# Optimization experiments

Hardware: AMD Instinct MI355X
Metric: run time of the kernel (lower is better)

The kernel has to match this reference:

```python
import jax, jax.numpy as jnp
import numpy as np

B, C, H, W = 2, 128, 48, 48
NUM_HEADS = 8


def dct_matrix(N):
    # Orthonormal DCT-II matrix: D[k, n] = s_k * cos(pi * (n + 0.5) * k / N)
    n = np.arange(N)
    D = np.cos(np.pi * (n[None, :] + 0.5) * n[:, None] / N) * np.sqrt(2.0 / N)
    D[0] *= 1.0 / np.sqrt(2.0)
    return jnp.asarray(D, dtype=jnp.float32)


def setup_inputs() -> dict:
    key = jax.random.key(0)
    ks = jax.random.split(key, 10)
    w_scale = 1.0 / np.sqrt(C)  # kaiming-ish init for 1x1 convs
    inp = {
        "freq_feat": jax.random.normal(ks[0], (B, C, H, W), dtype=jnp.float32),
        "spatial_feat": jax.random.normal(ks[1], (B, C, H, W), dtype=jnp.float32),
        "Wq": jax.random.normal(ks[2], (C, C), dtype=jnp.float32) * w_scale,
        "bq": jnp.zeros((C,), dtype=jnp.float32),
        "Wk": jax.random.normal(ks[3], (C, C), dtype=jnp.float32) * w_scale,
        "bk": jnp.zeros((C,), dtype=jnp.float32),
        "Wv": jax.random.normal(ks[4], (C, C), dtype=jnp.float32) * w_scale,
        "bv": jnp.zeros((C,), dtype=jnp.float32),
        "Wo": jax.random.normal(ks[5], (C, C), dtype=jnp.float32) * w_scale,
        "bo": jnp.zeros((C,), dtype=jnp.float32),
    }
    return inp


def _proj(x, Wm, b):
    # 1x1 conv == channel-mixing GEMM
    return jnp.einsum('oc,bchw->bohw', Wm, x) + b[None, :, None, None]


def reference(freq_feat, spatial_feat, Wq, bq, Wk, bk, Wv, bv, Wo, bo):
    b, c, h, w = freq_feat.shape
    nh = NUM_HEADS
    d = c // nh
    L = h * w

    # 2D orthonormal DCT-II of the spatial features
    DH = dct_matrix(h)
    DW = dct_matrix(w)
    spatial_freq = jnp.einsum('hm,bcmn,wn->bchw', DH, spatial_feat, DW)

    Q = _proj(freq_feat, Wq, bq)
    K = _proj(spatial_freq, Wk, bk)
    V = _proj(spatial_freq, Wv, bv)

    # (B, C, H, W) -> (B, nh, L, d)
    def to_heads(x):
        return x.reshape(b, nh, d, L).transpose(0, 1, 3, 2)

    Qh, Kh, Vh = to_heads(Q), to_heads(K), to_heads(V)

    scale = 1.0 / np.sqrt(d)
    scores = jnp.einsum('bhld,bhsd->bhls', Qh, Kh) * scale  # (B, nh, L, L)
    attn = jax.nn.softmax(scores, axis=-1)
    out = jnp.einsum('bhls,bhsd->bhld', attn, Vh)  # (B, nh, L, d)

    out = out.transpose(0, 1, 3, 2).reshape(b, c, h, w)
    return _proj(out, Wo, bo)
```

## Files before the change

### kernel.cpp

```cpp
#include <hip/hip_runtime.h>
#include <math.h>

#define L_TOT 2304
#define C_TOT 128
#define KSCALE 0.36067376022224085f

#if __has_builtin(__builtin_amdgcn_exp2f)
#define EXP2(x) __builtin_amdgcn_exp2f(x)
#else
#define EXP2(x) __expf(0.69314718055994531f * (x))
#endif

typedef float v4f  __attribute__((ext_vector_type(4)));
typedef __bf16 v8bf __attribute__((ext_vector_type(8)));
typedef __bf16 v4bf __attribute__((ext_vector_type(4)));

#define MFMA_16x16x32_BF16(A, B, C) __builtin_amdgcn_mfma_f32_16x16x32_bf16((A), (B), (C), 0, 0, 0)

__device__ __forceinline__ void async_cp16(const __bf16* g, __bf16* l){
  __builtin_amdgcn_global_load_lds((const __attribute__((address_space(1))) unsigned int*)g,
                                   (__attribute__((address_space(3))) unsigned int*)l,
                                   16, 0, 0);
}

#if __has_builtin(__builtin_amdgcn_permlane32_swap)
__device__ __forceinline__ void pl32swap(unsigned &a, unsigned &b){
  auto r = __builtin_amdgcn_permlane32_swap((int)a, (int)b, false, false);
  a = (unsigned)r[0]; b = (unsigned)r[1];
}
#else
__device__ __forceinline__ void pl32swap(unsigned &a, unsigned &b){
  asm volatile("v_permlane32_swap_b32 %0, %1" : "+v"(a), "+v"(b));
}
#endif
#if __has_builtin(__builtin_amdgcn_permlane16_swap)
__device__ __forceinline__ void pl16swap(unsigned &a, unsigned &b){
  auto r = __builtin_amdgcn_permlane16_swap((int)a, (int)b, false, false);
  a = (unsigned)r[0]; b = (unsigned)r[1];
}
#else
__device__ __forceinline__ void pl16swap(unsigned &a, unsigned &b){
  asm volatile("v_permlane16_swap_b32 %0, %1" : "+v"(a), "+v"(b));
}
#endif

template<int MODE>
__device__ __forceinline__ void mfma_proj(const float* __restrict__ W,
                                          const float* __restrict__ bias,
                                          const float* __restrict__ Xb,
                                          __bf16* __restrict__ Yh,
                                          float scale, float bscale,
                                          int n0, __bf16* Bhi, int tid){
  __bf16* Blo = Bhi + 4352;
  const int wave = tid >> 6, lane = tid & 63, qd = lane >> 4, cn = lane & 15;
  const int m0 = wave * 32;
  v8bf ahi[2][4], alo[2][4];
  #pragma unroll
  for (int rt = 0; rt < 2; rt++)
    #pragma unroll
    for (int ks = 0; ks < 4; ks++){
      const float* wp = W + (size_t)(m0 + rt * 16 + cn) * C_TOT + ks * 32 + qd * 8;
      float4 w0 = *(const float4*)wp;
      float4 w1 = *(const float4*)(wp + 4);
      float wv[8] = {w0.x, w0.y, w0.z, w0.w, w1.x, w1.y, w1.z, w1.w};
      #pragma unroll
      for (int j = 0; j < 8; j++){
        __bf16 h = (__bf16)wv[j];
        ahi[rt][ks][j] = h;
        alo[rt][ks][j] = (__bf16)(wv[j] - (float)h);
      }
    }
  {
    int k = tid >> 1, nh = tid & 1;
    const float* xp = Xb + (size_t)k * L_TOT + n0 + nh * 16;
    float4 x0 = *(const float4*)xp;
    float4 x1 = *(const float4*)(xp + 4);
    float4 x2 = *(const float4*)(xp + 8);
    float4 x3 = *(const float4*)(xp + 12);
    float xv[16] = {x0.x, x0.y, x0.z, x0.w, x1.x, x1.y, x1.z, x1.w,
                    x2.x, x2.y, x2.z, x2.w, x3.x, x3.y, x3.z, x3.w};
    #pragma unroll
    for (int i = 0; i < 16; i++){
      __bf16 h = (__bf16)xv[i];
      int row = nh * 16 + i;
      Bhi[row * 136 + k] = h;
      Blo[row * 136 + k] = (__bf16)(xv[i] - (float)h);
    }
  }
  __syncthreads();
  v4f acc[2][2];
  #pragma unroll
  for (int rt = 0; rt < 2; rt++)
    #pragma unroll
    for (int ct = 0; ct < 2; ct++) acc[rt][ct] = (v4f){0.f, 0.f, 0.f, 0.f};
  #pragma unroll
  for (int ks = 0; ks < 4; ks++){
    v8bf bhi[2], blo[2];
    #pragma unroll
    for (int ct = 0; ct < 2; ct++){
      bhi[ct] = *(const v8bf*)&Bhi[(ct * 16 + cn) * 136 + ks * 32 + qd * 8];
      blo[ct] = *(const v8bf*)&Blo[(ct * 16 + cn) * 136 + ks * 32 + qd * 8];
    }
    #pragma unroll
    for (int rt = 0; rt < 2; rt++)
      #pragma unroll
      for (int ct = 0; ct < 2; ct++){
        acc[rt][ct] = MFMA_16x16x32_BF16(ahi[rt][ks], bhi[ct], acc[rt][ct]);
        acc[rt][ct] = MFMA_16x16x32_BF16(ahi[rt][ks], blo[ct], acc[rt][ct]);
        acc[rt][ct] = MFMA_16x16x32_BF16(alo[rt][ks], bhi[ct], acc[rt][ct]);
      }
  }
  #pragma unroll
  for (int rt = 0; rt < 2; rt++){
    float bv[4];
    #pragma unroll
    for (int r = 0; r < 4; r++) bv[r] = bias[m0 + rt * 16 + qd * 4 + r] * bscale;
    #pragma unroll
    for (int ct = 0; ct < 2; ct++){
      int col = n0 + ct * 16 + cn;
      if (MODE == 1){
        v4bf kk;
        #pragma unroll
        for (int r = 0; r < 4; r++) kk[r] = (__bf16)((acc[rt][ct][r] + bv[r]) * scale);
        *(v4bf*)&Yh[(size_t)col * C_TOT + m0 + rt * 16 + qd * 4] = kk;
      } else {
        #pragma unroll
        for (int r = 0; r < 4; r++)
          Yh[(size_t)(m0 + rt * 16 + qd * 4 + r) * L_TOT + col] = (__bf16)(acc[rt][ct][r] + bv[r]);
      }
    }
  }
}

__global__ __launch_bounds__(256) void k_q_dct(
    const float* __restrict__ freq, const float* __restrict__ spat,
    const float* __restrict__ Wq, const float* __restrict__ bq,
    __bf16* __restrict__ QT, float* __restrict__ SF){
  __shared__ __align__(16) unsigned char smraw[34560];
  int tid = threadIdx.x;
  if (blockIdx.x < 144){
    int idx = blockIdx.x;
    int b = idx / 72, n0 = (idx % 72) * 32;
    size_t off = (size_t)b * C_TOT * L_TOT;
    mfma_proj<1>(Wq, bq, freq + off, QT + (size_t)b * L_TOT * C_TOT, 1.0f, 1.0f, n0, (__bf16*)smraw, tid);
    return;
  }
  int img = blockIdx.x - 144;
  __bf16* Xhi = (__bf16*)smraw;
  __bf16* Xlo = Xhi + 3456;
  __bf16* Dm  = Xhi + 6912;
  __bf16* Thi = Xhi + 10368;
  __bf16* Tlo = Xhi + 13824;
  const float* src = spat + (size_t)img * 2304;
  for (int i = tid; i < 8640; i += 256) ((unsigned int*)smraw)[i] = 0u;
  __syncthreads();
  for (int i = tid; i < 2304; i += 256){
    int a = i / 48, n = i - a * 48;
    int m = ((2 * n + 1) * a) % 192;
    float v = cosf(0.032724923474893679f * (float)m) * 0.204124145231931508f;
    if (a == 0) v *= 0.707106781186547524f;
    Dm[a * 72 + n] = (__bf16)v;
  }
  for (int i = tid; i < 2304; i += 256){
    int mm = i / 48, n = i - mm * 48;
    float v = src[i];
    __bf16 h = (__bf16)v;
    Xhi[mm * 72 + n] = h;
    Xlo[mm * 72 + n] = (__bf16)(v - (float)h);
  }
  __syncthreads();
  int wave = tid >> 6, lane = tid & 63, qd = lane >> 4, cn = lane & 15;
  for (int t = wave; t < 9; t += 4){
    int mi = t / 3, wi = t - mi * 3;
    v8bf ah0 = *(const v8bf*)&Xhi[(mi * 16 + cn) * 72 + qd * 8];
    v8bf ah1 = *(const v8bf*)&Xhi[(mi * 16 + cn) * 72 + 32 + qd * 8];
    v8bf al0 = *(const v8bf*)&Xlo[(mi * 16 + cn) * 72 + qd * 8];
    v8bf al1 = *(const v8bf*)&Xlo[(mi * 16 + cn) * 72 + 32 + qd * 8];
    v8bf b0 = *(const v8bf*)&Dm[(wi * 16 + cn) * 72 + qd * 8];
    v8bf b1 = *(const v8bf*)&Dm[(wi * 16 + cn) * 72 + 32 + qd * 8];
    v4f acc = (v4f){0.f, 0.f, 0.f, 0.f};
    acc = MFMA_16x16x32_BF16(ah0, b0, acc);
    acc = MFMA_16x16x32_BF16(ah1, b1, acc);
    acc = MFMA_16x16x32_BF16(al0, b0, acc);
    acc = MFMA_16x16x32_BF16(al1, b1, acc);
    v4bf th, tl;
    #pragma unroll
    for (int r = 0; r < 4; r++){
      __bf16 h = (__bf16)acc[r];
      th[r] = h;
      tl[r] = (__bf16)(acc[r] - (float)h);
    }
    *(v4bf*)&Thi[(wi * 16 + cn) * 72 + mi * 16 + qd * 4] = th;
    *(v4bf*)&Tlo[(wi * 16 + cn) * 72 + mi * 16 + qd * 4] = tl;
  }
  __syncthreads();
  float* dst = SF + (size_t)img * 2304;
  for (int t = wave; t < 9; t += 4){
    int hi_ = t / 3, wi = t - hi_ * 3;
    v8bf a0 = *(const v8bf*)&Dm[(hi_ * 16 + cn) * 72 + qd * 8];
    v8bf a1 = *(const v8bf*)&Dm[(hi_ * 16 + cn) * 72 + 32 + qd * 8];
    v8bf bh0 = *(const v8bf*)&Thi[(wi * 16 + cn) * 72 + qd * 8];
    v8bf bh1 = *(const v8bf*)&Thi[(wi * 16 + cn) * 72 + 32 + qd * 8];
    v8bf bl0 = *(const v8bf*)&Tlo[(wi * 16 + cn) * 72 + qd * 8];
    v8bf bl1 = *(const v8bf*)&Tlo[(wi * 16 + cn) * 72 + 32 + qd * 8];
    v4f acc = (v4f){0.f, 0.f, 0.f, 0.f};
    acc = MFMA_16x16x32_BF16(a0, bh0, acc);
    acc = MFMA_16x16x32_BF16(a1, bh1, acc);
    acc = MFMA_16x16x32_BF16(a0, bl0, acc);
    acc = MFMA_16x16x32_BF16(a1, bl1, acc);
    int w = wi * 16 + cn;
    #pragma unroll
    for (int r = 0; r < 4; r++)
      dst[(size_t)(hi_ * 16 + qd * 4 + r) * 48 + w] = acc[r];
  }
}

__global__ __launch_bounds__(256) void k_kv(
    const float* __restrict__ SF,
    const float* __restrict__ Wk, const float* __restrict__ bk,
    const float* __restrict__ Wv, const float* __restrict__ bv,
    __bf16* __restrict__ KT, __bf16* __restrict__ Vg){
  __shared__ __align__(16) unsigned char smraw[17408];
  int job = blockIdx.x / 144;
  int idx = blockIdx.x % 144;
  int b = idx / 72, n0 = (idx % 72) * 32;
  size_t off = (size_t)b * C_TOT * L_TOT;
  if (job == 0)
    mfma_proj<1>(Wk, bk, SF + off, KT + (size_t)b * L_TOT * C_TOT, KSCALE, 1.0f, n0, (__bf16*)smraw, threadIdx.x);
  else
    mfma_proj<2>(Wv, bv, SF + off, Vg + off, 1.0f, 1.0f, n0, (__bf16*)smraw, threadIdx.x);
}

__global__ __launch_bounds__(256) void k_attn(const __bf16* __restrict__ QT,
                                              const __bf16* __restrict__ KT,
                                              const __bf16* __restrict__ V,
                                              __bf16* __restrict__ AO){
  const int L = L_TOT;
  int bh = blockIdx.y;
  int b = bh >> 3, h = bh & 7;
  int c0 = h * 16;
  const __bf16* QTb = QT + (size_t)b * L * C_TOT;
  const __bf16* KTb = KT + (size_t)b * L * C_TOT;
  const __bf16* Vb  = V  + ((size_t)b * C_TOT + c0) * L;
  int tid = threadIdx.x;
  int wave = tid >> 6, lane = tid & 63;
  int qd = lane >> 4, cn = lane & 15;
  int l0 = blockIdx.x * 48;

  __shared__ __align__(16) __bf16 smem[8192 + 8192];
  __bf16* Kt = smem;
  __bf16* Vs = smem + 8192;

  v8bf qf[3];
  #pragma unroll
  for (int t = 0; t < 3; t++){
    #pragma unroll
    for (int j = 0; j < 8; j++) qf[t][j] = (__bf16)0.0f;
  }
  if (qd < 2){
    #pragma unroll
    for (int t = 0; t < 3; t++)
      qf[t] = *(const v8bf*)&QTb[(size_t)(l0 + t * 16 + cn) * C_TOT + c0 + qd * 8];
  }

  v4f acc[3];
  float den[3] = {0.f, 0.f, 0.f};
  #pragma unroll
  for (int t = 0; t < 3; t++) acc[t] = (v4f){0.f, 0.f, 0.f, 0.f};

  for (int ch = 0; ch < 5; ch++){
    int s0 = ch * 512;
    int cnt = (ch == 4) ? 256 : 512;
    __syncthreads();
    {
      int per = (cnt >> 5) >> 2;
      for (int jj = 0; jj < per; jj++){
        int j = wave * per + jj;
        int s = j * 32 + (lane >> 1);
        async_cp16(KTb + (size_t)(s0 + s) * C_TOT + c0 + (lane & 1) * 8,
                   Kt + j * 512);
      }
      if (cnt == 512){
        #pragma unroll
        for (int jj = 0; jj < 4; jj++){
          int d = wave * 4 + jj;
          async_cp16(Vb + (size_t)d * L + s0 + ((lane ^ (d & 7)) << 3),
                     Vs + d * 512);
        }
      } else {
        int d = tid >> 4, og = tid & 15;
        const __bf16* gp = Vb + (size_t)d * L + s0 + og * 16;
        v8bf v0 = *(const v8bf*)gp;
        v8bf v1 = *(const v8bf*)(gp + 8);
        int pd = d & 7;
        *(v8bf*)&Vs[d * 512 + (((og * 2)     ^ pd) << 3)] = v0;
        *(v8bf*)&Vs[d * 512 + (((og * 2 + 1) ^ pd) << 3)] = v1;
      }
    }
    __syncthreads();

    int nsu = cnt >> 7;
    int wbase = wave * (cnt >> 2);
    for (int su = 0; su < nsu; su++){
      int sb = wbase + su * 32;
      v8bf a0, a1;
      #pragma unroll
      for (int j = 0; j < 8; j++){ a0[j] = (__bf16)0.0f; a1[j] = (__bf16)0.0f; }
      if (qd < 2){
        a0 = *(const v8bf*)&Kt[(sb + cn) * 16 + qd * 8];
        a1 = *(const v8bf*)&Kt[(sb + 16 + cn) * 16 + qd * 8];
      }
      int jv = sb >> 3;
      v8bf vf = *(const v8bf*)&Vs[cn * 512 + (((jv + qd) ^ (cn & 7)) << 3)];
      #pragma unroll
      for (int t = 0; t < 3; t++){
        v4f z = {0.f, 0.f, 0.f, 0.f};
        v4f st0 = MFMA_16x16x32_BF16(a0, qf[t], z);
        v4f st1 = MFMA_16x16x32_BF16(a1, qf[t], z);
        float p0[4], p1[4];
        #pragma unroll
        for (int i = 0; i < 4; i++){
          p0[i] = EXP2(st0[i]); den[t] += p0[i];
          p1[i] = EXP2(st1[i]); den[t] += p1[i];
        }
        v4bf cc0, cc1;
        #pragma unroll
        for (int i = 0; i < 4; i++){ cc0[i] = (__bf16)p0[i]; cc1[i] = (__bf16)p1[i]; }
        unsigned U0 = ((unsigned*)&cc0)[0], U1 = ((unsigned*)&cc0)[1];
        unsigned U2 = ((unsigned*)&cc1)[0], U3 = ((unsigned*)&cc1)[1];
        pl32swap(U0, U2); pl32swap(U1, U3);
        pl16swap(U0, U2); pl16swap(U1, U3);
        v8bf pf;
        ((unsigned*)&pf)[0] = U0; ((unsigned*)&pf)[1] = U1;
        ((unsigned*)&pf)[2] = U2; ((unsigned*)&pf)[3] = U3;
        acc[t] = MFMA_16x16x32_BF16(vf, pf, acc[t]);
      }
    }
  }

  __syncthreads();
  float* redA = (float*)smem;
  float* redD = (float*)smem + 3072;
  #pragma unroll
  for (int t = 0; t < 3; t++){
    *(v4f*)&redA[((wave * 3 + t) * 64 + lane) * 4] = acc[t];
    redD[(wave * 3 + t) * 64 + lane] = den[t];
  }
  __syncthreads();
  if (wave < 3){
    int t = wave;
    v4f a = (v4f){0.f, 0.f, 0.f, 0.f};
    float dn = 0.f;
    #pragma unroll
    for (int w2 = 0; w2 < 4; w2++){
      v4f xx = *(const v4f*)&redA[((w2 * 3 + t) * 64 + lane) * 4];
      a[0] += xx[0]; a[1] += xx[1]; a[2] += xx[2]; a[3] += xx[3];
      dn += redD[(w2 * 3 + t) * 64 + lane];
    }
    dn += __shfl_xor(dn, 16);
    dn += __shfl_xor(dn, 32);
    float inv = 1.0f / dn;
    __bf16* Ao = AO + ((size_t)b * C_TOT + c0) * L;
    #pragma unroll
    for (int r2 = 0; r2 < 4; r2++)
      Ao[(size_t)(qd * 4 + r2) * L + l0 + t * 16 + cn] = (__bf16)(a[r2] * inv);
  }
}

__global__ __launch_bounds__(256) void k_oproj(const __bf16* __restrict__ AO,
                                               const float* __restrict__ Wo, const float* __restrict__ bo,
                                               float* __restrict__ out){
  __shared__ __align__(16) __bf16 Bs[32 * 136];
  int b = blockIdx.y, n0 = blockIdx.x * 32;
  int tid = threadIdx.x;
  const int wave = tid >> 6, lane = tid & 63, qd = lane >> 4, cn = lane & 15;
  const int m0 = wave * 32;
  v8bf ahi[2][4], alo[2][4];
  #pragma unroll
  for (int rt = 0; rt < 2; rt++)
    #pragma unroll
    for (int ks = 0; ks < 4; ks++){
      const float* wp = Wo + (size_t)(m0 + rt * 16 + cn) * C_TOT + ks * 32 + qd * 8;
      float4 w0 = *(const float4*)wp;
      float4 w1 = *(const float4*)(wp + 4);
      float wv[8] = {w0.x, w0.y, w0.z, w0.w, w1.x, w1.y, w1.z, w1.w};
      #pragma unroll
      for (int j = 0; j < 8; j++){
        __bf16 h = (__bf16)wv[j];
        ahi[rt][ks][j] = h;
        alo[rt][ks][j] = (__bf16)(wv[j] - (float)h);
      }
    }
  {
    int k = tid >> 1, nh = tid & 1;
    const __bf16* src = AO + ((size_t)b * C_TOT + k) * L_TOT + n0 + nh * 16;
    v8bf x0 = *(const v8bf*)src;
    v8bf x1 = *(const v8bf*)(src + 8);
    #pragma unroll
    for (int i = 0; i < 8; i++){
      Bs[(nh * 16 + i) * 136 + k] = x0[i];
      Bs[(nh * 16 + 8 + i) * 136 + k] = x1[i];
    }
  }
  __syncthreads();
  v4f acc[2][2];
  #pragma unroll
  for (int rt = 0; rt < 2; rt++)
    #pragma unroll
    for (int ct = 0; ct < 2; ct++) acc[rt][ct] = (v4f){0.f, 0.f, 0.f, 0.f};
  #pragma unroll
  for (int ks = 0; ks < 4; ks++){
    v8bf bf[2];
    #pragma unroll
    for (int ct = 0; ct < 2; ct++)
      bf[ct] = *(const v8bf*)&Bs[(ct * 16 + cn) * 136 + ks * 32 + qd * 8];
    #pragma unroll
    for (int rt = 0; rt < 2; rt++)
      #pragma unroll
      for (int ct = 0; ct < 2; ct++){
        acc[rt][ct] = MFMA_16x16x32_BF16(ahi[rt][ks], bf[ct], acc[rt][ct]);
        acc[rt][ct] = MFMA_16x16x32_BF16(alo[rt][ks], bf[ct], acc[rt][ct]);
      }
  }
  float* ob = out + (size_t)b * C_TOT * L_TOT;
  #pragma unroll
  for (int rt = 0; rt < 2; rt++){
    float bv[4];
    #pragma unroll
    for (int r = 0; r < 4; r++) bv[r] = bo[m0 + rt * 16 + qd * 4 + r];
    #pragma unroll
    for (int ct = 0; ct < 2; ct++){
      int col = n0 + ct * 16 + cn;
      #pragma unroll
      for (int r = 0; r < 4; r++)
        ob[(size_t)(m0 + rt * 16 + qd * 4 + r) * L_TOT + col] = acc[rt][ct][r] + bv[r];
    }
  }
}

extern "C" void kernel_launch(void* const* d_in, const int* in_sizes, int n_in,
                              void* d_out, int out_size, void* d_ws, size_t ws_size,
                              hipStream_t stream){
  const float* freq = (const float*)d_in[0];
  const float* spat = (const float*)d_in[1];
  const float* Wq = (const float*)d_in[2]; const float* bq = (const float*)d_in[3];
  const float* Wk = (const float*)d_in[4]; const float* bk = (const float*)d_in[5];
  const float* Wv = (const float*)d_in[6]; const float* bv = (const float*)d_in[7];
  const float* Wo = (const float*)d_in[8]; const float* bo = (const float*)d_in[9];
  __bf16* base = (__bf16*)d_ws;

  __bf16* QTg = base;
  __bf16* KTg = base + 589824;
  __bf16* Vg  = base + 1179648;
  __bf16* AOg = base + 1769472;
  float*  SFg = (float*)(base + 2359296);
  float* out = (float*)d_out;

  k_q_dct<<<dim3(400), dim3(256), 0, stream>>>(freq, spat, Wq, bq, QTg, SFg);
  k_kv<<<dim3(288), dim3(256), 0, stream>>>(SFg, Wk, bk, Wv, bv, KTg, Vg);
  k_attn<<<dim3(48, 16), dim3(256), 0, stream>>>(QTg, KTg, Vg, AOg);
  k_oproj<<<dim3(72, 2), dim3(256), 0, stream>>>(AOg, Wo, bo, out);
}
```

Measured before the change: 115.8 us.

## Fuse all stages into one persistent kernel with grid barriers

Replaces the four separate launches (Q projection plus DCT, K/V projection, attention, output projection) with a single 768-block kernel. Stages are separated by atomic-counter grid barriers, and per-tile counters let the last attention block that finishes a column group run the output projection for it. The intent is to remove launch overhead and the inter-kernel drain/fill gaps. In exchange it needs all 768 blocks to be co-resident, which the launch bounds ask for at 3 blocks per CU, or it deadlocks. It also adds a memset and spin-wait costs.

Result: slower. 334.8 us (+189.2%).

```diff
diff --git a/kernel.cpp b/kernel.cpp
--- a/kernel.cpp
+++ b/kernel.cpp
@@ -43,6 +43,16 @@
   asm volatile("v_permlane16_swap_b32 %0, %1" : "+v"(a), "+v"(b));
 }
 #endif
+
+__device__ __forceinline__ void gbar(unsigned* c, unsigned target){
+  __syncthreads();
+  if (threadIdx.x == 0){
+    __hip_atomic_fetch_add(c, 1u, __ATOMIC_RELEASE, __HIP_MEMORY_SCOPE_AGENT);
+    while (__hip_atomic_load(c, __ATOMIC_ACQUIRE, __HIP_MEMORY_SCOPE_AGENT) < target)
+      __builtin_amdgcn_s_sleep(8);
+  }
+  __syncthreads();
+}
 
 template<int MODE>
 __device__ __forceinline__ void mfma_proj(const float* __restrict__ W,
@@ -132,26 +142,14 @@
   }
 }
 
-__global__ __launch_bounds__(256) void k_q_dct(
-    const float* __restrict__ freq, const float* __restrict__ spat,
-    const float* __restrict__ Wq, const float* __restrict__ bq,
-    __bf16* __restrict__ QT, float* __restrict__ SF){
-  __shared__ __align__(16) unsigned char smraw[34560];
-  int tid = threadIdx.x;
-  if (blockIdx.x < 144){
-    int idx = blockIdx.x;
-    int b = idx / 72, n0 = (idx % 72) * 32;
-    size_t off = (size_t)b * C_TOT * L_TOT;
-    mfma_proj<1>(Wq, bq, freq + off, QT + (size_t)b * L_TOT * C_TOT, 1.0f, 1.0f, n0, (__bf16*)smraw, tid);
-    return;
-  }
-  int img = blockIdx.x - 144;
+__device__ __forceinline__ void dct_img(const float* __restrict__ src,
+                                        float* __restrict__ dst,
+                                        unsigned char* smraw, int tid){
   __bf16* Xhi = (__bf16*)smraw;
   __bf16* Xlo = Xhi + 3456;
   __bf16* Dm  = Xhi + 6912;
   __bf16* Thi = Xhi + 10368;
   __bf16* Tlo = Xhi + 13824;
-  const float* src = spat + (size_t)img * 2304;
   for (int i = tid; i < 8640; i += 256) ((unsigned int*)smraw)[i] = 0u;
   __syncthreads();
   for (int i = tid; i < 2304; i += 256){
@@ -194,7 +192,6 @@
     *(v4bf*)&Tlo[(wi * 16 + cn) * 72 + mi * 16 + qd * 4] = tl;
   }
   __syncthreads();
-  float* dst = SF + (size_t)img * 2304;
   for (int t = wave; t < 9; t += 4){
     int hi_ = t / 3, wi = t - hi_ * 3;
     v8bf a0 = *(const v8bf*)&Dm[(hi_ * 16 + cn) * 72 + qd * 8];
@@ -215,41 +212,126 @@
   }
 }
 
-__global__ __launch_bounds__(256) void k_kv(
-    const float* __restrict__ SF,
+__device__ __forceinline__ void oproj_dev(const __bf16* __restrict__ AO,
+                                          const float* __restrict__ Wo,
+                                          const float* __restrict__ bo,
+                                          float* __restrict__ out,
+                                          int b, int n0, __bf16* Bs, int tid){
+  __syncthreads();
+  const int wave = tid >> 6, lane = tid & 63, qd = lane >> 4, cn = lane & 15;
+  const int m0 = wave * 32;
+  v8bf ahi[2][4], alo[2][4];
+  #pragma unroll
+  for (int rt = 0; rt < 2; rt++)
+    #pragma unroll
+    for (int ks = 0; ks < 4; ks++){
+      const float* wp = Wo + (size_t)(m0 + rt * 16 + cn) * C_TOT + ks * 32 + qd * 8;
+      float4 w0 = *(const float4*)wp;
+      float4 w1 = *(const float4*)(wp + 4);
+      float wv[8] = {w0.x, w0.y, w0.z, w0.w, w1.x, w1.y, w1.z, w1.w};
+      #pragma unroll
+      for (int j = 0; j < 8; j++){
+        __bf16 h = (__bf16)wv[j];
+        ahi[rt][ks][j] = h;
+        alo[rt][ks][j] = (__bf16)(wv[j] - (float)h);
+      }
+    }
+  {
+    int k = tid >> 1, nh = tid & 1;
+    const __bf16* src = AO + ((size_t)b * C_TOT + k) * L_TOT + n0 + nh * 16;
+    v8bf x0 = *(const v8bf*)src;
+    v8bf x1 = *(const v8bf*)(src + 8);
+    #pragma unroll
+    for (int i = 0; i < 8; i++){
+      Bs[(nh * 16 + i) * 136 + k] = x0[i];
+      Bs[(nh * 16 + 8 + i) * 136 + k] = x1[i];
+    }
+  }
+  __syncthreads();
+  v4f acc[2][2];
+  #pragma unroll
+  for (int rt = 0; rt < 2; rt++)
+    #pragma unroll
+    for (int ct = 0; ct < 2; ct++) acc[rt][ct] = (v4f){0.f, 0.f, 0.f, 0.f};
+  #pragma unroll
+  for (int ks = 0; ks < 4; ks++){
+    v8bf bf[2];
+    #pragma unroll
+    for (int ct = 0; ct < 2; ct++)
+      bf[ct] = *(const v8bf*)&Bs[(ct * 16 + cn) * 136 + ks * 32 + qd * 8];
+    #pragma unroll
+    for (int rt = 0; rt < 2; rt++)
+      #pragma unroll
+      for (int ct = 0; ct < 2; ct++){
+        acc[rt][ct] = MFMA_16x16x32_BF16(ahi[rt][ks], bf[ct], acc[rt][ct]);
+        acc[rt][ct] = MFMA_16x16x32_BF16(alo[rt][ks], bf[ct], acc[rt][ct]);
+      }
+  }
+  float* ob = out + (size_t)b * C_TOT * L_TOT;
+  #pragma unroll
+  for (int rt = 0; rt < 2; rt++){
+    float bv[4];
+    #pragma unroll
+    for (int r = 0; r < 4; r++) bv[r] = bo[m0 + rt * 16 + qd * 4 + r];
+    #pragma unroll
+    for (int ct = 0; ct < 2; ct++){
+      int col = n0 + ct * 16 + cn;
+      #pragma unroll
+      for (int r = 0; r < 4; r++)
+        ob[(size_t)(m0 + rt * 16 + qd * 4 + r) * L_TOT + col] = acc[rt][ct][r] + bv[r];
+    }
+  }
+}
+
+__global__ __launch_bounds__(256, 3) void k_mega(
+    const float* __restrict__ freq, const float* __restrict__ spat,
+    const float* __restrict__ Wq, const float* __restrict__ bq,
     const float* __restrict__ Wk, const float* __restrict__ bk,
     const float* __restrict__ Wv, const float* __restrict__ bv,
-    __bf16* __restrict__ KT, __bf16* __restrict__ Vg){
-  __shared__ __align__(16) unsigned char smraw[17408];
-  int job = blockIdx.x / 144;
-  int idx = blockIdx.x % 144;
-  int b = idx / 72, n0 = (idx % 72) * 32;
-  size_t off = (size_t)b * C_TOT * L_TOT;
-  if (job == 0)
-    mfma_proj<1>(Wk, bk, SF + off, KT + (size_t)b * L_TOT * C_TOT, KSCALE, 1.0f, n0, (__bf16*)smraw, threadIdx.x);
-  else
-    mfma_proj<2>(Wv, bv, SF + off, Vg + off, 1.0f, 1.0f, n0, (__bf16*)smraw, threadIdx.x);
-}
-
-__global__ __launch_bounds__(256) void k_attn(const __bf16* __restrict__ QT,
-                                              const __bf16* __restrict__ KT,
-                                              const __bf16* __restrict__ V,
-                                              __bf16* __restrict__ AO){
+    const float* __restrict__ Wo, const float* __restrict__ bo,
+    __bf16* __restrict__ QT, __bf16* __restrict__ KT, __bf16* __restrict__ Vg,
+    __bf16* __restrict__ AO, float* __restrict__ SF,
+    unsigned* __restrict__ cnt, float* __restrict__ out){
+  __shared__ __align__(16) unsigned char SMEM[34816];
+  __shared__ int oflag[2];
+  const int bid = blockIdx.x, tid = threadIdx.x;
+
+  if (bid < 144){
+    int b = bid / 72, n0 = (bid % 72) * 32;
+    size_t off = (size_t)b * C_TOT * L_TOT;
+    mfma_proj<1>(Wq, bq, freq + off, QT + (size_t)b * L_TOT * C_TOT,
+                 1.0f, 1.0f, n0, (__bf16*)SMEM, tid);
+  } else if (bid < 400){
+    int img = bid - 144;
+    dct_img(spat + (size_t)img * 2304, SF + (size_t)img * 2304, SMEM, tid);
+  }
+  gbar(&cnt[0], 768u);
+
+  if (bid < 288){
+    int job = bid / 144, idx = bid % 144;
+    int b = idx / 72, n0 = (idx % 72) * 32;
+    size_t off = (size_t)b * C_TOT * L_TOT;
+    if (job == 0)
+      mfma_proj<1>(Wk, bk, SF + off, KT + (size_t)b * L_TOT * C_TOT,
+                   KSCALE, 1.0f, n0, (__bf16*)SMEM, tid);
+    else
+      mfma_proj<2>(Wv, bv, SF + off, Vg + off, 1.0f, 1.0f, n0, (__bf16*)SMEM, tid);
+  }
+  gbar(&cnt[1], 768u);
+
   const int L = L_TOT;
-  int bh = blockIdx.y;
-  int b = bh >> 3, h = bh & 7;
-  int c0 = h * 16;
+  const int l0b = bid % 48, bh = bid / 48;
+  const int b = bh >> 3, h = bh & 7;
+  const int c0 = h * 16;
   const __bf16* QTb = QT + (size_t)b * L * C_TOT;
   const __bf16* KTb = KT + (size_t)b * L * C_TOT;
-  const __bf16* Vb  = V  + ((size_t)b * C_TOT + c0) * L;
-  int tid = threadIdx.x;
-  int wave = tid >> 6, lane = tid & 63;
-  int qd = lane >> 4, cn = lane & 15;
-  int l0 = blockIdx.x * 48;
-
-  __shared__ __align__(16) __bf16 smem[8192 + 8192];
-  __bf16* Kt = smem;
-  __bf16* Vs = smem + 8192;
+  const __bf16* Vb  = Vg + ((size_t)b * C_TOT + c0) * L;
+  const int wave = tid >> 6, lane = tid & 63;
+  const int qd = lane >> 4, cn = lane & 15;
+  const int l0 = l0b * 48;
+
+  __bf16* Kt = (__bf16*)SMEM;
+  __bf16* Vs = (__bf16*)SMEM + 8192;
 
   v8bf qf[3];
   #pragma unroll
@@ -270,17 +352,17 @@
 
   for (int ch = 0; ch < 5; ch++){
     int s0 = ch * 512;
-    int cnt = (ch == 4) ? 256 : 512;
+    int cnt_k = (ch == 4) ? 256 : 512;
     __syncthreads();
     {
-      int per = (cnt >> 5) >> 2;
+      int per = (cnt_k >> 5) >> 2;
       for (int jj = 0; jj < per; jj++){
         int j = wave * per + jj;
         int s = j * 32 + (lane >> 1);
         async_cp16(KTb + (size_t)(s0 + s) * C_TOT + c0 + (lane & 1) * 8,
                    Kt + j * 512);
       }
-      if (cnt == 512){
+      if (cnt_k == 512){
         #pragma unroll
         for (int jj = 0; jj < 4; jj++){
           int d = wave * 4 + jj;
@@ -299,8 +381,8 @@
     }
     __syncthreads();
 
-    int nsu = cnt >> 7;
-    int wbase = wave * (cnt >> 2);
+    int nsu = cnt_k >> 7;
+    int wbase = wave * (cnt_k >> 2);
     for (int su = 0; su < nsu; su++){
       int sb = wbase + su * 32;
       v8bf a0, a1;
@@ -339,8 +421,8 @@
   }
 
   __syncthreads();
-  float* redA = (float*)smem;
-  float* redD = (float*)smem + 3072;
+  float* redA = (float*)SMEM;
+  float* redD = (float*)SMEM + 3072;
   #pragma unroll
   for (int t = 0; t < 3; t++){
     *(v4f*)&redA[((wave * 3 + t) * 64 + lane) * 4] = acc[t];
@@ -365,76 +447,26 @@
     for (int r2 = 0; r2 < 4; r2++)
       Ao[(size_t)(qd * 4 + r2) * L + l0 + t * 16 + cn] = (__bf16)(a[r2] * inv);
   }
-}
-
-__global__ __launch_bounds__(256) void k_oproj(const __bf16* __restrict__ AO,
-                                               const float* __restrict__ Wo, const float* __restrict__ bo,
-                                               float* __restrict__ out){
-  __shared__ __align__(16) __bf16 Bs[32 * 136];
-  int b = blockIdx.y, n0 = blockIdx.x * 32;
-  int tid = threadIdx.x;
-  const int wave = tid >> 6, lane = tid & 63, qd = lane >> 4, cn = lane & 15;
-  const int m0 = wave * 32;
-  v8bf ahi[2][4], alo[2][4];
-  #pragma unroll
-  for (int rt = 0; rt < 2; rt++)
-    #pragma unroll
-    for (int ks = 0; ks < 4; ks++){
-      const float* wp = Wo + (size_t)(m0 + rt * 16 + cn) * C_TOT + ks * 32 + qd * 8;
-      float4 w0 = *(const float4*)wp;
-      float4 w1 = *(const float4*)(wp + 4);
-      float wv[8] = {w0.x, w0.y, w0.z, w0.w, w1.x, w1.y, w1.z, w1.w};
-      #pragma unroll
-      for (int j = 0; j < 8; j++){
-        __bf16 h = (__bf16)wv[j];
-        ahi[rt][ks][j] = h;
-        alo[rt][ks][j] = (__bf16)(wv[j] - (float)h);
-      }
-    }
-  {
-    int k = tid >> 1, nh = tid & 1;
-    const __bf16* src = AO + ((size_t)b * C_TOT + k) * L_TOT + n0 + nh * 16;
-    v8bf x0 = *(const v8bf*)src;
-    v8bf x1 = *(const v8bf*)(src + 8);
-    #pragma unroll
-    for (int i = 0; i < 8; i++){
-      Bs[(nh * 16 + i) * 136 + k] = x0[i];
-      Bs[(nh * 16 + 8 + i) * 136 + k] = x1[i];
-    }
-  }
-  __syncthreads();
-  v4f acc[2][2];
-  #pragma unroll
-  for (int rt = 0; rt < 2; rt++)
-    #pragma unroll
-    for (int ct = 0; ct < 2; ct++) acc[rt][ct] = (v4f){0.f, 0.f, 0.f, 0.f};
-  #pragma unroll
-  for (int ks = 0; ks < 4; ks++){
-    v8bf bf[2];
-    #pragma unroll
-    for (int ct = 0; ct < 2; ct++)
-      bf[ct] = *(const v8bf*)&Bs[(ct * 16 + cn) * 136 + ks * 32 + qd * 8];
-    #pragma unroll
-    for (int rt = 0; rt < 2; rt++)
-      #pragma unroll
-      for (int ct = 0; ct < 2; ct++){
-        acc[rt][ct] = MFMA_16x16x32_BF16(ahi[rt][ks], bf[ct], acc[rt][ct]);
-        acc[rt][ct] = MFMA_16x16x32_BF16(alo[rt][ks], bf[ct], acc[rt][ct]);
-      }
-  }
-  float* ob = out + (size_t)b * C_TOT * L_TOT;
-  #pragma unroll
-  for (int rt = 0; rt < 2; rt++){
-    float bv[4];
-    #pragma unroll
-    for (int r = 0; r < 4; r++) bv[r] = bo[m0 + rt * 16 + qd * 4 + r];
-    #pragma unroll
-    for (int ct = 0; ct < 2; ct++){
-      int col = n0 + ct * 16 + cn;
-      #pragma unroll
-      for (int r = 0; r < 4; r++)
-        ob[(size_t)(m0 + rt * 16 + qd * 4 + r) * L_TOT + col] = acc[rt][ct][r] + bv[r];
-    }
+
+  __syncthreads();
+  if (tid == 0){
+    int g0 = (3 * l0b) >> 1;
+    oflag[0] = -1; oflag[1] = -1;
+    #pragma unroll
+    for (int k = 0; k < 2; k++){
+      int g = g0 + k;
+      unsigned tgt = ((g % 3) == 1) ? 16u : 8u;
+      unsigned old = __hip_atomic_fetch_add(&cnt[2 + b * 72 + g], 1u,
+                                            __ATOMIC_ACQ_REL, __HIP_MEMORY_SCOPE_AGENT);
+      if (old + 1u == tgt) oflag[k] = g;
+    }
+  }
+  __syncthreads();
+  #pragma unroll
+  for (int k = 0; k < 2; k++){
+    int g = oflag[k];
+    if (g >= 0)
+      oproj_dev(AO, Wo, bo, out, b, g * 32, (__bf16*)SMEM, tid);
   }
 }
 
@@ -454,10 +486,10 @@
   __bf16* Vg  = base + 1179648;
   __bf16* AOg = base + 1769472;
   float*  SFg = (float*)(base + 2359296);
+  unsigned* cnt = (unsigned*)((char*)d_ws + 7340032);
   float* out = (float*)d_out;
 
-  k_q_dct<<<dim3(400), dim3(256), 0, stream>>>(freq, spat, Wq, bq, QTg, SFg);
-  k_kv<<<dim3(288), dim3(256), 0, stream>>>(SFg, Wk, bk, Wv, bv, KTg, Vg);
-  k_attn<<<dim3(48, 16), dim3(256), 0, stream>>>(QTg, KTg, Vg, AOg);
-  k_oproj<<<dim3(72, 2), dim3(256), 0, stream>>>(AOg, Wo, bo, out);
-}
+  hipMemsetAsync(cnt, 0, 1024, stream);
+  k_mega<<<dim3(768), dim3(256), 0, stream>>>(freq, spat, Wq, bq, Wk, bk, Wv, bv,
+                                              Wo, bo, QTg, KTg, Vg, AOg, SFg, cnt, out);
+}
```

## Fuse output projection into attention kernel via atomic completion counters

Applied to the files above, without the earlier changes.

Removes the separate output-projection launch. Each attention block increments per-column-group atomic counters once it has written its AO tile. The last block to finish a 32-column group then runs the output projection for that group in its epilogue. The counters are zeroed in the first kernel. This saves a kernel launch and its tail, but it adds atomics, extra serial work for the finishing blocks, and relies on acquire/release ordering for the AO data to be visible.

Result: slower. 155.6 us (+34.4%).

```diff
diff --git a/kernel.cpp b/kernel.cpp
--- a/kernel.cpp
+++ b/kernel.cpp
@@ -135,9 +135,11 @@
 __global__ __launch_bounds__(256) void k_q_dct(
     const float* __restrict__ freq, const float* __restrict__ spat,
     const float* __restrict__ Wq, const float* __restrict__ bq,
-    __bf16* __restrict__ QT, float* __restrict__ SF){
+    __bf16* __restrict__ QT, float* __restrict__ SF,
+    unsigned* __restrict__ cnt){
   __shared__ __align__(16) unsigned char smraw[34560];
   int tid = threadIdx.x;
+  if (blockIdx.x == 0 && tid < 160) cnt[tid] = 0u;
   if (blockIdx.x < 144){
     int idx = blockIdx.x;
     int b = idx / 72, n0 = (idx % 72) * 32;
@@ -231,10 +233,85 @@
     mfma_proj<2>(Wv, bv, SF + off, Vg + off, 1.0f, 1.0f, n0, (__bf16*)smraw, threadIdx.x);
 }
 
+__device__ __forceinline__ void oproj_dev(const __bf16* __restrict__ AO,
+                                          const float* __restrict__ Wo,
+                                          const float* __restrict__ bo,
+                                          float* __restrict__ out,
+                                          int b, int n0, __bf16* Bs, int tid){
+  __syncthreads();
+  const int wave = tid >> 6, lane = tid & 63, qd = lane >> 4, cn = lane & 15;
+  const int m0 = wave * 32;
+  v8bf ahi[2][4], alo[2][4];
+  #pragma unroll
+  for (int rt = 0; rt < 2; rt++)
+    #pragma unroll
+    for (int ks = 0; ks < 4; ks++){
+      const float* wp = Wo + (size_t)(m0 + rt * 16 + cn) * C_TOT + ks * 32 + qd * 8;
+      float4 w0 = *(const float4*)wp;
+      float4 w1 = *(const float4*)(wp + 4);
+      float wv[8] = {w0.x, w0.y, w0.z, w0.w, w1.x, w1.y, w1.z, w1.w};
+      #pragma unroll
+      for (int j = 0; j < 8; j++){
+        __bf16 h = (__bf16)wv[j];
+        ahi[rt][ks][j] = h;
+        alo[rt][ks][j] = (__bf16)(wv[j] - (float)h);
+      }
+    }
+  {
+    int k = tid >> 1, nh = tid & 1;
+    const __bf16* src = AO + ((size_t)b * C_TOT + k) * L_TOT + n0 + nh * 16;
+    v8bf x0 = *(const v8bf*)src;
+    v8bf x1 = *(const v8bf*)(src + 8);
+    #pragma unroll
+    for (int i = 0; i < 8; i++){
+      Bs[(nh * 16 + i) * 136 + k] = x0[i];
+      Bs[(nh * 16 + 8 + i) * 136 + k] = x1[i];
+    }
+  }
+  __syncthreads();
+  v4f acc[2][2];
+  #pragma unroll
+  for (int rt = 0; rt < 2; rt++)
+    #pragma unroll
+    for (int ct = 0; ct < 2; ct++) acc[rt][ct] = (v4f){0.f, 0.f, 0.f, 0.f};
+  #pragma unroll
+  for (int ks = 0; ks < 4; ks++){
+    v8bf bf[2];
+    #pragma unroll
+    for (int ct = 0; ct < 2; ct++)
+      bf[ct] = *(const v8bf*)&Bs[(ct * 16 + cn) * 136 + ks * 32 + qd * 8];
+    #pragma unroll
+    for (int rt = 0; rt < 2; rt++)
+      #pragma unroll
+      for (int ct = 0; ct < 2; ct++){
+        acc[rt][ct] = MFMA_16x16x32_BF16(ahi[rt][ks], bf[ct], acc[rt][ct]);
+        acc[rt][ct] = MFMA_16x16x32_BF16(alo[rt][ks], bf[ct], acc[rt][ct]);
+      }
+  }
+  float* ob = out + (size_t)b * C_TOT * L_TOT;
+  #pragma unroll
+  for (int rt = 0; rt < 2; rt++){
+    float bv[4];
+    #pragma unroll
+    for (int r = 0; r < 4; r++) bv[r] = bo[m0 + rt * 16 + qd * 4 + r];
+    #pragma unroll
+    for (int ct = 0; ct < 2; ct++){
+      int col = n0 + ct * 16 + cn;
+      #pragma unroll
+      for (int r = 0; r < 4; r++)
+        ob[(size_t)(m0 + rt * 16 + qd * 4 + r) * L_TOT + col] = acc[rt][ct][r] + bv[r];
+    }
+  }
+}
+
 __global__ __launch_bounds__(256) void k_attn(const __bf16* __restrict__ QT,
                                               const __bf16* __restrict__ KT,
                                               const __bf16* __restrict__ V,
-                                              __bf16* __restrict__ AO){
+                                              __bf16* __restrict__ AO,
+                                              const float* __restrict__ Wo,
+                                              const float* __restrict__ bo,
+                                              unsigned* __restrict__ cnt,
+                                              float* __restrict__ out){
   const int L = L_TOT;
   int bh = blockIdx.y;
   int b = bh >> 3, h = bh & 7;
@@ -245,9 +322,11 @@
   int tid = threadIdx.x;
   int wave = tid >> 6, lane = tid & 63;
   int qd = lane >> 4, cn = lane & 15;
-  int l0 = blockIdx.x * 48;
+  int l0b = blockIdx.x;
+  int l0 = l0b * 48;
 
   __shared__ __align__(16) __bf16 smem[8192 + 8192];
+  __shared__ int oflag[2];
   __bf16* Kt = smem;
   __bf16* Vs = smem + 8192;
 
@@ -270,17 +349,17 @@
 
   for (int ch = 0; ch < 5; ch++){
     int s0 = ch * 512;
-    int cnt = (ch == 4) ? 256 : 512;
+    int cnt_k = (ch == 4) ? 256 : 512;
     __syncthreads();
     {
-      int per = (cnt >> 5) >> 2;
+      int per = (cnt_k >> 5) >> 2;
       for (int jj = 0; jj < per; jj++){
         int j = wave * per + jj;
         int s = j * 32 + (lane >> 1);
         async_cp16(KTb + (size_t)(s0 + s) * C_TOT + c0 + (lane & 1) * 8,
                    Kt + j * 512);
       }
-      if (cnt == 512){
+      if (cnt_k == 512){
         #pragma unroll
         for (int jj = 0; jj < 4; jj++){
           int d = wave * 4 + jj;
@@ -299,8 +378,8 @@
     }
     __syncthreads();
 
-    int nsu = cnt >> 7;
-    int wbase = wave * (cnt >> 2);
+    int nsu = cnt_k >> 7;
+    int wbase = wave * (cnt_k >> 2);
     for (int su = 0; su < nsu; su++){
       int sb = wbase + su * 32;
       v8bf a0, a1;
@@ -365,76 +444,26 @@
     for (int r2 = 0; r2 < 4; r2++)
       Ao[(size_t)(qd * 4 + r2) * L + l0 + t * 16 + cn] = (__bf16)(a[r2] * inv);
   }
-}
-
-__global__ __launch_bounds__(256) void k_oproj(const __bf16* __restrict__ AO,
-                                               const float* __restrict__ Wo, const float* __restrict__ bo,
-                                               float* __restrict__ out){
-  __shared__ __align__(16) __bf16 Bs[32 * 136];
-  int b = blockIdx.y, n0 = blockIdx.x * 32;
-  int tid = threadIdx.x;
-  const int wave = tid >> 6, lane = tid & 63, qd = lane >> 4, cn = lane & 15;
-  const int m0 = wave * 32;
-  v8bf ahi[2][4], alo[2][4];
-  #pragma unroll
-  for (int rt = 0; rt < 2; rt++)
-    #pragma unroll
-    for (int ks = 0; ks < 4; ks++){
-      const float* wp = Wo + (size_t)(m0 + rt * 16 + cn) * C_TOT + ks * 32 + qd * 8;
-      float4 w0 = *(const float4*)wp;
-      float4 w1 = *(const float4*)(wp + 4);
-      float wv[8] = {w0.x, w0.y, w0.z, w0.w, w1.x, w1.y, w1.z, w1.w};
-      #pragma unroll
-      for (int j = 0; j < 8; j++){
-        __bf16 h = (__bf16)wv[j];
-        ahi[rt][ks][j] = h;
-        alo[rt][ks][j] = (__bf16)(wv[j] - (float)h);
-      }
-    }
-  {
-    int k = tid >> 1, nh = tid & 1;
-    const __bf16* src = AO + ((size_t)b * C_TOT + k) * L_TOT + n0 + nh * 16;
-    v8bf x0 = *(const v8bf*)src;
-    v8bf x1 = *(const v8bf*)(src + 8);
-    #pragma unroll
-    for (int i = 0; i < 8; i++){
-      Bs[(nh * 16 + i) * 136 + k] = x0[i];
-      Bs[(nh * 16 + 8 + i) * 136 + k] = x1[i];
-    }
-  }
-  __syncthreads();
-  v4f acc[2][2];
-  #pragma unroll
-  for (int rt = 0; rt < 2; rt++)
-    #pragma unroll
-    for (int ct = 0; ct < 2; ct++) acc[rt][ct] = (v4f){0.f, 0.f, 0.f, 0.f};
-  #pragma unroll
-  for (int ks = 0; ks < 4; ks++){
-    v8bf bf[2];
-    #pragma unroll
-    for (int ct = 0; ct < 2; ct++)
-      bf[ct] = *(const v8bf*)&Bs[(ct * 16 + cn) * 136 + ks * 32 + qd * 8];
-    #pragma unroll
-    for (int rt = 0; rt < 2; rt++)
-      #pragma unroll
-      for (int ct = 0; ct < 2; ct++){
-        acc[rt][ct] = MFMA_16x16x32_BF16(ahi[rt][ks], bf[ct], acc[rt][ct]);
-        acc[rt][ct] = MFMA_16x16x32_BF16(alo[rt][ks], bf[ct], acc[rt][ct]);
-      }
-  }
-  float* ob = out + (size_t)b * C_TOT * L_TOT;
-  #pragma unroll
-  for (int rt = 0; rt < 2; rt++){
-    float bv[4];
-    #pragma unroll
-    for (int r = 0; r < 4; r++) bv[r] = bo[m0 + rt * 16 + qd * 4 + r];
-    #pragma unroll
-    for (int ct = 0; ct < 2; ct++){
-      int col = n0 + ct * 16 + cn;
-      #pragma unroll
-      for (int r = 0; r < 4; r++)
-        ob[(size_t)(m0 + rt * 16 + qd * 4 + r) * L_TOT + col] = acc[rt][ct][r] + bv[r];
-    }
+
+  __syncthreads();
+  if (tid == 0){
+    int g0 = (3 * l0b) >> 1;
+    oflag[0] = -1; oflag[1] = -1;
+    #pragma unroll
+    for (int k = 0; k < 2; k++){
+      int g = g0 + k;
+      unsigned tgt = ((g % 3) == 1) ? 16u : 8u;
+      unsigned old = __hip_atomic_fetch_add(&cnt[2 + b * 72 + g], 1u,
+                                            __ATOMIC_ACQ_REL, __HIP_MEMORY_SCOPE_AGENT);
+      if (old + 1u == tgt) oflag[k] = g;
+    }
+  }
+  __syncthreads();
+  #pragma unroll
+  for (int k = 0; k < 2; k++){
+    int g = oflag[k];
+    if (g >= 0)
+      oproj_dev(AO, Wo, bo, out, b, g * 32, (__bf16*)smem, tid);
   }
 }
 
@@ -454,10 +483,10 @@
   __bf16* Vg  = base + 1179648;
   __bf16* AOg = base + 1769472;
   float*  SFg = (float*)(base + 2359296);
+  unsigned* cnt = (unsigned*)((char*)d_ws + 7340032);
   float* out = (float*)d_out;
 
-  k_q_dct<<<dim3(400), dim3(256), 0, stream>>>(freq, spat, Wq, bq, QTg, SFg);
+  k_q_dct<<<dim3(400), dim3(256), 0, stream>>>(freq, spat, Wq, bq, QTg, SFg, cnt);
   k_kv<<<dim3(288), dim3(256), 0, stream>>>(SFg, Wk, bk, Wv, bv, KTg, Vg);
-  k_attn<<<dim3(48, 16), dim3(256), 0, stream>>>(QTg, KTg, Vg, AOg);
-  k_oproj<<<dim3(72, 2), dim3(256), 0, stream>>>(AOg, Wo, bo, out);
-}
+  k_attn<<<dim3(48, 16), dim3(256), 0, stream>>>(QTg, KTg, Vg, AOg, Wo, bo, cnt, out);
+}
```

## Double-buffer K/V chunks in attention kernel to overlap loads with MFMA

Applied to the files above, without the earlier changes.

Replaces the five single-buffered 512-key chunks with nine 256-key chunks held in two shared-memory buffers. While one chunk is being computed, the next K chunk is fetched asynchronously and the next V chunk is loaded into registers, then written to shared memory after the compute. This drops one barrier per chunk and hides global-load latency behind the exp/MFMA work. The cost is smaller chunks, more loop iterations, and more register pressure from holding the prefetched V values.

New measurement: 113.6 us. No clear change (-1.9%).

```diff
diff --git a/kernel.cpp b/kernel.cpp
--- a/kernel.cpp
+++ b/kernel.cpp
@@ -247,9 +247,7 @@
   int qd = lane >> 4, cn = lane & 15;
   int l0 = blockIdx.x * 48;
 
-  __shared__ __align__(16) __bf16 smem[8192 + 8192];
-  __bf16* Kt = smem;
-  __bf16* Vs = smem + 8192;
+  __shared__ __align__(16) __bf16 smem[16384];
 
   v8bf qf[3];
   #pragma unroll
@@ -268,40 +266,46 @@
   #pragma unroll
   for (int t = 0; t < 3; t++) acc[t] = (v4f){0.f, 0.f, 0.f, 0.f};
 
-  for (int ch = 0; ch < 5; ch++){
-    int s0 = ch * 512;
-    int cnt = (ch == 4) ? 256 : 512;
-    __syncthreads();
-    {
-      int per = (cnt >> 5) >> 2;
-      for (int jj = 0; jj < per; jj++){
-        int j = wave * per + jj;
+  const int vd = tid >> 4, vog = tid & 15, vpd = vd & 7;
+
+  {
+    #pragma unroll
+    for (int jj = 0; jj < 2; jj++){
+      int j = wave * 2 + jj;
+      int s = j * 32 + (lane >> 1);
+      async_cp16(KTb + (size_t)s * C_TOT + c0 + (lane & 1) * 8, smem + j * 512);
+    }
+    const __bf16* gp = Vb + (size_t)vd * L + vog * 16;
+    v8bf v0 = *(const v8bf*)gp;
+    v8bf v1 = *(const v8bf*)(gp + 8);
+    *(v8bf*)&smem[8192 + vd * 256 + (((vog * 2)     ^ vpd) << 3)] = v0;
+    *(v8bf*)&smem[8192 + vd * 256 + (((vog * 2 + 1) ^ vpd) << 3)] = v1;
+  }
+  __syncthreads();
+
+  int cur = 0;
+  for (int ch = 0; ch < 9; ch++){
+    int nxt = cur ^ 1;
+    v8bf v0, v1;
+    if (ch < 8){
+      int s0n = (ch + 1) * 256;
+      #pragma unroll
+      for (int jj = 0; jj < 2; jj++){
+        int j = wave * 2 + jj;
         int s = j * 32 + (lane >> 1);
-        async_cp16(KTb + (size_t)(s0 + s) * C_TOT + c0 + (lane & 1) * 8,
-                   Kt + j * 512);
-      }
-      if (cnt == 512){
-        #pragma unroll
-        for (int jj = 0; jj < 4; jj++){
-          int d = wave * 4 + jj;
-          async_cp16(Vb + (size_t)d * L + s0 + ((lane ^ (d & 7)) << 3),
-                     Vs + d * 512);
-        }
-      } else {
-        int d = tid >> 4, og = tid & 15;
-        const __bf16* gp = Vb + (size_t)d * L + s0 + og * 16;
-        v8bf v0 = *(const v8bf*)gp;
-        v8bf v1 = *(const v8bf*)(gp + 8);
-        int pd = d & 7;
-        *(v8bf*)&Vs[d * 512 + (((og * 2)     ^ pd) << 3)] = v0;
-        *(v8bf*)&Vs[d * 512 + (((og * 2 + 1) ^ pd) << 3)] = v1;
-      }
-    }
-    __syncthreads();
-
-    int nsu = cnt >> 7;
-    int wbase = wave * (cnt >> 2);
-    for (int su = 0; su < nsu; su++){
+        async_cp16(KTb + (size_t)(s0n + s) * C_TOT + c0 + (lane & 1) * 8,
+                   smem + nxt * 4096 + j * 512);
+      }
+      const __bf16* gp = Vb + (size_t)vd * L + s0n + vog * 16;
+      v0 = *(const v8bf*)gp;
+      v1 = *(const v8bf*)(gp + 8);
+    }
+
+    const __bf16* Kt = smem + cur * 4096;
+    const __bf16* Vs = smem + 8192 + cur * 4096;
+    int wbase = wave * 64;
+    #pragma unroll
+    for (int su = 0; su < 2; su++){
       int sb = wbase + su * 32;
       v8bf a0, a1;
       #pragma unroll
@@ -311,7 +315,7 @@
         a1 = *(const v8bf*)&Kt[(sb + 16 + cn) * 16 + qd * 8];
       }
       int jv = sb >> 3;
-      v8bf vf = *(const v8bf*)&Vs[cn * 512 + (((jv + qd) ^ (cn & 7)) << 3)];
+      v8bf vf = *(const v8bf*)&Vs[cn * 256 + (((jv + qd) ^ (cn & 7)) << 3)];
       #pragma unroll
       for (int t = 0; t < 3; t++){
         v4f z = {0.f, 0.f, 0.f, 0.f};
@@ -336,9 +340,15 @@
         acc[t] = MFMA_16x16x32_BF16(vf, pf, acc[t]);
       }
     }
-  }
-
-  __syncthreads();
+
+    if (ch < 8){
+      *(v8bf*)&smem[8192 + nxt * 4096 + vd * 256 + (((vog * 2)     ^ vpd) << 3)] = v0;
+      *(v8bf*)&smem[8192 + nxt * 4096 + vd * 256 + (((vog * 2 + 1) ^ vpd) << 3)] = v1;
+    }
+    __syncthreads();
+    cur = nxt;
+  }
+
   float* redA = (float*)smem;
   float* redD = (float*)smem + 3072;
   #pragma unroll
```
